# Performance work log

Measured on AMD Instinct MI355X. Metric: run time of the kernel, lower is better.

## Reference

```python
import jax, jax.numpy as jnp
import numpy as np

TARGET_DIM, DRUG_DIM, INT_DIM, HID = 1024, 128, 128, 32
LN_EPS = 1e-5  # torch nn.LayerNorm default (module's eps arg is unused for LN)


def _layernorm(x, g, b):
    mu = jnp.mean(x, axis=-1, keepdims=True)
    var = jnp.var(x, axis=-1, keepdims=True)
    return (x - mu) * jax.lax.rsqrt(var + LN_EPS) * g + b


def setup_inputs() -> dict:
    key = jax.random.key(0)
    ks = jax.random.split(key, 10)
    B, NR, NA = 4, 512, 64
    s_t = 1.0 / np.sqrt(TARGET_DIM)
    s_d = 1.0 / np.sqrt(DRUG_DIM)
    s_o = 1.0 / np.sqrt(HID * HID)
    return {
        "target_embedding": jax.random.normal(ks[0], (B, NR, TARGET_DIM), jnp.float32),
        "drug_embedding": jax.random.normal(ks[1], (B, NA, DRUG_DIM), jnp.float32),
        "target_mask": jnp.ones((B, NR), jnp.float32),
        "drug_mask": jnp.ones((B, NA), jnp.float32),
        "ln_t_g": jnp.ones((TARGET_DIM,), jnp.float32),
        "ln_t_b": jnp.zeros((TARGET_DIM,), jnp.float32),
        "ln_d_g": jnp.ones((DRUG_DIM,), jnp.float32),
        "ln_d_b": jnp.zeros((DRUG_DIM,), jnp.float32),
        "W_t": jax.random.uniform(ks[2], (HID, TARGET_DIM), jnp.float32, -s_t, s_t),
        "b_t": jax.random.uniform(ks[3], (HID,), jnp.float32, -s_t, s_t),
        "W_d": jax.random.uniform(ks[4], (HID, DRUG_DIM), jnp.float32, -s_d, s_d),
        "b_d": jax.random.uniform(ks[5], (HID,), jnp.float32, -s_d, s_d),
        "W_out": jax.random.uniform(ks[6], (INT_DIM, HID * HID), jnp.float32, -s_o, s_o),
        "b_out": jax.random.uniform(ks[7], (INT_DIM,), jnp.float32, -s_o, s_o),
    }


def reference(target_embedding, drug_embedding, target_mask, drug_mask,
              ln_t_g, ln_t_b, ln_d_g, ln_d_b, W_t, b_t, W_d, b_d, W_out, b_out):
    t = _layernorm(target_embedding, ln_t_g, ln_t_b)
    d = _layernorm(drug_embedding, ln_d_g, ln_d_b)
    # projections + mask: [B,NR,H], [B,NA,H]
    tf = (t @ W_t.T + b_t) * target_mask[..., None]
    df = (d @ W_d.T + b_d) * drug_mask[..., None]
    # fused outer-product + linear_out: W_out row index i over flat (c*H+e)
    W3 = W_out.reshape(INT_DIM, HID, HID)  # [i, c, e]
    outer = jnp.einsum('bnc,bme,ice->bnmi', tf, df, W3) + b_out
    mask = target_mask[:, :, None] * drug_mask[:, None, :]  # [B,NR,NA]
    outer = outer * mask[..., None]
    return outer, mask
```

## Files before the change

kernel.cpp:

```cpp
#include <hip/hip_runtime.h>

typedef __attribute__((ext_vector_type(8))) short short8;
typedef __attribute__((ext_vector_type(4))) float f32x4;

#define LNP_YSTRIDE 1032
#define GSTR 1048

__device__ __forceinline__ unsigned short f2bf(float f) {
  union { float f; unsigned u; } v; v.f = f;
  unsigned r = v.u + 0x7FFFu + ((v.u >> 16) & 1u);
  return (unsigned short)(r >> 16);
}
__device__ __forceinline__ unsigned pack2(float a, float b) {
  return (unsigned)f2bf(a) | ((unsigned)f2bf(b) << 16);
}
__device__ __forceinline__ short8 packW(float4 a, float4 b) {
  union { short8 s; unsigned u[4]; } r;
  r.u[0] = pack2(a.x, a.y); r.u[1] = pack2(a.z, a.w);
  r.u[2] = pack2(b.x, b.y); r.u[3] = pack2(b.z, b.w);
  return r.s;
}

template<int ROWLEN>
__device__ __forceinline__ void lnproj(
    const float* __restrict__ X, const float* __restrict__ g, const float* __restrict__ bia,
    const float* __restrict__ W, const float* __restrict__ pb, const float* __restrict__ msk,
    unsigned short* __restrict__ outb, int row0, unsigned short* Yl, float* pd, int tid)
{
  const int w = tid >> 6, lid = tid & 63, l = tid & 15, q = (tid >> 4) & 3;

  #pragma unroll
  for (int rr = 0; rr < 4; ++rr) {
    const int row = w * 4 + rr;
    const float* xr = X + (size_t)(row0 + row) * ROWLEN;
    if (ROWLEN == 1024) {
      float4 v[4];
      float s = 0.f, s2 = 0.f;
      #pragma unroll
      for (int k = 0; k < 4; ++k) {
        v[k] = *(const float4*)(xr + 4 * lid + 256 * k);
        s  += (v[k].x + v[k].y) + (v[k].z + v[k].w);
        s2 += (v[k].x * v[k].x + v[k].y * v[k].y) + (v[k].z * v[k].z + v[k].w * v[k].w);
      }
      #pragma unroll
      for (int off = 32; off >= 1; off >>= 1) { s += __shfl_xor(s, off, 64); s2 += __shfl_xor(s2, off, 64); }
      const float mu = s * (1.f / 1024.f);
      const float rs = rsqrtf(s2 * (1.f / 1024.f) - mu * mu + 1e-5f);
      #pragma unroll
      for (int k = 0; k < 4; ++k) {
        float4 gg = *(const float4*)(g + 4 * lid + 256 * k);
        float4 bb = *(const float4*)(bia + 4 * lid + 256 * k);
        float y0 = (v[k].x - mu) * rs * gg.x + bb.x;
        float y1 = (v[k].y - mu) * rs * gg.y + bb.y;
        float y2 = (v[k].z - mu) * rs * gg.z + bb.z;
        float y3 = (v[k].w - mu) * rs * gg.w + bb.w;
        unsigned* yd = (unsigned*)(Yl + row * LNP_YSTRIDE + 4 * lid + 256 * k);
        yd[0] = pack2(y0, y1); yd[1] = pack2(y2, y3);
      }
    } else {
      float2 v = *(const float2*)(xr + 2 * lid);
      float s = v.x + v.y, s2 = v.x * v.x + v.y * v.y;
      #pragma unroll
      for (int off = 32; off >= 1; off >>= 1) { s += __shfl_xor(s, off, 64); s2 += __shfl_xor(s2, off, 64); }
      const float mu = s * (1.f / 128.f);
      const float rs = rsqrtf(s2 * (1.f / 128.f) - mu * mu + 1e-5f);
      float2 gg = *(const float2*)(g + 2 * lid);
      float2 bb = *(const float2*)(bia + 2 * lid);
      *(unsigned*)(Yl + row * LNP_YSTRIDE + 2 * lid) =
          pack2((v.x - mu) * rs * gg.x + bb.x, (v.y - mu) * rs * gg.y + bb.y);
    }
  }
  __syncthreads();

  const int KST = ROWLEN / 32;
  const int ht = w & 1, kh = w >> 1;
  const int h = ht * 16 + l;
  f32x4 acc = {0.f, 0.f, 0.f, 0.f};
  #pragma unroll
  for (int s = kh * (KST / 2); s < kh * (KST / 2) + KST / 2; ++s) {
    short8 af = *(const short8*)(Yl + l * LNP_YSTRIDE + s * 32 + q * 8);
    const float* wp = W + (size_t)h * ROWLEN + s * 32 + q * 8;
    short8 bf = packW(*(const float4*)wp, *(const float4*)(wp + 4));
    acc = __builtin_amdgcn_mfma_f32_16x16x32_bf16(af, bf, acc, 0, 0, 0);
  }
  if (w >= 2) {
    #pragma unroll
    for (int r = 0; r < 4; ++r) pd[ht * 256 + (q * 4 + r) * 16 + l] = acc[r];
  }
  __syncthreads();
  if (w < 2) {
    const float pbv = pb[h];
    #pragma unroll
    for (int r = 0; r < 4; ++r) {
      const int rg = row0 + q * 4 + r;
      float val = acc[r] + pd[ht * 256 + (q * 4 + r) * 16 + l] + pbv;
      val *= msk[rg];
      outb[(size_t)rg * 32 + h] = f2bf(val);
    }
  }
}

__global__ __launch_bounds__(256) void k_pre(
    const float* __restrict__ tgt, const float* __restrict__ drg,
    const float* __restrict__ tmask, const float* __restrict__ dmask,
    const float* __restrict__ ln_t_g, const float* __restrict__ ln_t_b,
    const float* __restrict__ ln_d_g, const float* __restrict__ ln_d_b,
    const float* __restrict__ W_t, const float* __restrict__ b_t,
    const float* __restrict__ W_d, const float* __restrict__ b_d,
    const float* __restrict__ W_out,
    unsigned short* __restrict__ w3pp, unsigned short* __restrict__ tfb,
    unsigned short* __restrict__ dfb, float* __restrict__ mask_out)
{
  __shared__ unsigned short Yl[16 * LNP_YSTRIDE];
  __shared__ float pd[2 * 16 * 16];
  const int blk = blockIdx.x, tid = threadIdx.x;
  if (blk < 128) {
    lnproj<1024>(tgt, ln_t_g, ln_t_b, W_t, b_t, tmask, tfb, blk * 16, Yl, pd, tid);
  } else if (blk < 144) {
    lnproj<128>(drg, ln_d_g, ln_d_b, W_d, b_d, dmask, dfb, (blk - 128) * 16, Yl, pd, tid);
  } else if (blk < 152) {
    const int tg = (blk - 144) * 256 + tid;
    #pragma unroll
    for (int rep = 0; rep < 2; ++rep) {
      const int f = tg + rep * 2048;
      const int i = f >> 5, e = f & 31;
      unsigned short us[32];
      #pragma unroll
      for (int c = 0; c < 32; ++c) us[c] = f2bf(W_out[i * 1024 + c * 32 + e]);
      unsigned* dst = (unsigned*)(w3pp + (size_t)f * 32);
      #pragma unroll
      for (int j = 0; j < 16; ++j) dst[j] = (unsigned)us[2 * j] | ((unsigned)us[2 * j + 1] << 16);
    }
  } else {
    const int base = ((blk - 152) * 256 + tid) * 4;
    const int b = base >> 15;
    const float tm = tmask[base >> 6];
    float4 d = *(const float4*)(dmask + b * 64 + (base & 63));
    float4 o; o.x = tm * d.x; o.y = tm * d.y; o.z = tm * d.z; o.w = tm * d.w;
    *(float4*)(mask_out + base) = o;
  }
}

__global__ __launch_bounds__(256) void k_main(
    const unsigned short* __restrict__ w3pp, const unsigned short* __restrict__ tfb,
    const unsigned short* __restrict__ dfb, const float* __restrict__ b_out,
    const float* __restrict__ tmask, const float* __restrict__ dmask,
    float* __restrict__ out)
{
  __shared__ unsigned short Gl[16 * GSTR];
  const int id = blockIdx.x;
  const int b = id >> 7, n16 = (id >> 2) & 31, iq = id & 3;
  const int n0 = n16 * 16, i0 = iq * 32;
  const int tid = threadIdx.x, w = tid >> 6, l = tid & 15, q = (tid >> 4) & 3;

  short8 atf = *(const short8*)(tfb + (size_t)(b * 512 + n0 + l) * 32 + q * 8);
  short8 adf[4];
  #pragma unroll
  for (int mt = 0; mt < 4; ++mt)
    adf[mt] = *(const short8*)(dfb + (size_t)(b * 64 + mt * 16 + l) * 32 + q * 8);

  const f32x4 zero = {0.f, 0.f, 0.f, 0.f};

  for (int t = w * 16; t < w * 16 + 16; ++t) {
    const int f = i0 * 32 + t * 16 + l;
    short8 bw = *(const short8*)(w3pp + (size_t)f * 32 + q * 8);
    f32x4 d = __builtin_amdgcn_mfma_f32_16x16x32_bf16(atf, bw, zero, 0, 0, 0);
    const int floc = t * 16 + l, ip = floc >> 5, e = floc & 31;
    #pragma unroll
    for (int r = 0; r < 4; ++r)
      Gl[(q * 4 + r) * GSTR + ip * 32 + e] = f2bf(d[r]);
  }
  __syncthreads();

  const float bo0 = b_out[i0 + l], bo1 = b_out[i0 + 16 + l];

  for (int j = 0; j < 8; ++j) {
    const int p = w * 8 + j, n = p >> 1, it = p & 1;
    short8 bg = *(const short8*)(Gl + n * GSTR + (it * 16 + l) * 32 + q * 8);
    const float tmv = tmask[b * 512 + n0 + n];
    const float bo = it ? bo1 : bo0;
    const size_t obase = ((size_t)(b * 512 + n0 + n) * 64) * 128 + (size_t)(i0 + it * 16 + l);
    #pragma unroll
    for (int mt = 0; mt < 4; ++mt) {
      f32x4 d = __builtin_amdgcn_mfma_f32_16x16x32_bf16(adf[mt], bg, zero, 0, 0, 0);
      #pragma unroll
      for (int r = 0; r < 4; ++r) {
        const int m = mt * 16 + q * 4 + r;
        out[obase + (size_t)m * 128] = (d[r] + bo) * (tmv * dmask[b * 64 + m]);
      }
    }
  }
}

extern "C" void kernel_launch(void* const* d_in, const int* in_sizes, int n_in,
                              void* d_out, int out_size, void* d_ws, size_t ws_size,
                              hipStream_t stream)
{
  const float* tgt    = (const float*)d_in[0];
  const float* drg    = (const float*)d_in[1];
  const float* tmask  = (const float*)d_in[2];
  const float* dmask  = (const float*)d_in[3];
  const float* ln_t_g = (const float*)d_in[4];
  const float* ln_t_b = (const float*)d_in[5];
  const float* ln_d_g = (const float*)d_in[6];
  const float* ln_d_b = (const float*)d_in[7];
  const float* W_t    = (const float*)d_in[8];
  const float* b_t    = (const float*)d_in[9];
  const float* W_d    = (const float*)d_in[10];
  const float* b_d    = (const float*)d_in[11];
  const float* W_out  = (const float*)d_in[12];
  const float* b_out  = (const float*)d_in[13];

  float* out = (float*)d_out;
  float* mask_out = out + (size_t)4 * 512 * 64 * 128;

  char* ws = (char*)d_ws;
  unsigned short* w3pp = (unsigned short*)(ws);
  unsigned short* tfb  = (unsigned short*)(ws + 262144);
  unsigned short* dfb  = (unsigned short*)(ws + 262144 + 131072);

  k_pre<<<dim3(280), dim3(256), 0, stream>>>(
      tgt, drg, tmask, dmask, ln_t_g, ln_t_b, ln_d_g, ln_d_b,
      W_t, b_t, W_d, b_d, W_out, w3pp, tfb, dfb, mask_out);
  k_main<<<dim3(512), dim3(256), 0, stream>>>(
      w3pp, tfb, dfb, b_out, tmask, dmask, out);
}
```

Baseline: 116.5 us.

## Vectorize output stores via swapped MFMA operands and rebalance preprocessing blocks

The second-stage MFMA now takes the G tile as the A operand and the drug features as B. Each lane therefore holds four consecutive interaction outputs and writes them with one float4 store instead of four scalar strided stores, and b_out and dmask are loaded up front. The pre-kernel's LayerNorm+projection now handles 8 rows per block instead of 16, doubling the block count. The W_out repack is spread over 16 blocks, and the combined mask output moves into the main kernel. The aim is fewer store instructions on the dominant output write and better occupancy in the pre-kernel, at the cost of the MFMA computing 8 unused garbage rows per projection block.

Result: slower. 119.6 us (+2.6%).

```diff
diff --git a/kernel.cpp b/kernel.cpp
--- a/kernel.cpp
+++ b/kernel.cpp
@@ -3,7 +3,7 @@
 typedef __attribute__((ext_vector_type(8))) short short8;
 typedef __attribute__((ext_vector_type(4))) float f32x4;
 
-#define LNP_YSTRIDE 1032
+#define YSTR 1032
 #define GSTR 1048
 
 __device__ __forceinline__ unsigned short f2bf(float f) {
@@ -22,7 +22,7 @@
 }
 
 template<int ROWLEN>
-__device__ __forceinline__ void lnproj(
+__device__ __forceinline__ void lnproj8(
     const float* __restrict__ X, const float* __restrict__ g, const float* __restrict__ bia,
     const float* __restrict__ W, const float* __restrict__ pb, const float* __restrict__ msk,
     unsigned short* __restrict__ outb, int row0, unsigned short* Yl, float* pd, int tid)
@@ -30,8 +30,8 @@
   const int w = tid >> 6, lid = tid & 63, l = tid & 15, q = (tid >> 4) & 3;
 
   #pragma unroll
-  for (int rr = 0; rr < 4; ++rr) {
-    const int row = w * 4 + rr;
+  for (int rr = 0; rr < 2; ++rr) {
+    const int row = w * 2 + rr;
     const float* xr = X + (size_t)(row0 + row) * ROWLEN;
     if (ROWLEN == 1024) {
       float4 v[4];
@@ -50,12 +50,9 @@
       for (int k = 0; k < 4; ++k) {
         float4 gg = *(const float4*)(g + 4 * lid + 256 * k);
         float4 bb = *(const float4*)(bia + 4 * lid + 256 * k);
-        float y0 = (v[k].x - mu) * rs * gg.x + bb.x;
-        float y1 = (v[k].y - mu) * rs * gg.y + bb.y;
-        float y2 = (v[k].z - mu) * rs * gg.z + bb.z;
-        float y3 = (v[k].w - mu) * rs * gg.w + bb.w;
-        unsigned* yd = (unsigned*)(Yl + row * LNP_YSTRIDE + 4 * lid + 256 * k);
-        yd[0] = pack2(y0, y1); yd[1] = pack2(y2, y3);
+        unsigned* yd = (unsigned*)(Yl + row * YSTR + 4 * lid + 256 * k);
+        yd[0] = pack2((v[k].x - mu) * rs * gg.x + bb.x, (v[k].y - mu) * rs * gg.y + bb.y);
+        yd[1] = pack2((v[k].z - mu) * rs * gg.z + bb.z, (v[k].w - mu) * rs * gg.w + bb.w);
       }
     } else {
       float2 v = *(const float2*)(xr + 2 * lid);
@@ -66,7 +63,7 @@
       const float rs = rsqrtf(s2 * (1.f / 128.f) - mu * mu + 1e-5f);
       float2 gg = *(const float2*)(g + 2 * lid);
       float2 bb = *(const float2*)(bia + 2 * lid);
-      *(unsigned*)(Yl + row * LNP_YSTRIDE + 2 * lid) =
+      *(unsigned*)(Yl + row * YSTR + 2 * lid) =
           pack2((v.x - mu) * rs * gg.x + bb.x, (v.y - mu) * rs * gg.y + bb.y);
     }
   }
@@ -78,24 +75,23 @@
   f32x4 acc = {0.f, 0.f, 0.f, 0.f};
   #pragma unroll
   for (int s = kh * (KST / 2); s < kh * (KST / 2) + KST / 2; ++s) {
-    short8 af = *(const short8*)(Yl + l * LNP_YSTRIDE + s * 32 + q * 8);
+    short8 af = *(const short8*)(Yl + l * YSTR + s * 32 + q * 8);
     const float* wp = W + (size_t)h * ROWLEN + s * 32 + q * 8;
     short8 bf = packW(*(const float4*)wp, *(const float4*)(wp + 4));
     acc = __builtin_amdgcn_mfma_f32_16x16x32_bf16(af, bf, acc, 0, 0, 0);
   }
-  if (w >= 2) {
-    #pragma unroll
-    for (int r = 0; r < 4; ++r) pd[ht * 256 + (q * 4 + r) * 16 + l] = acc[r];
+  if (kh == 1 && q < 2) {
+    #pragma unroll
+    for (int r = 0; r < 4; ++r) pd[ht * 128 + (q * 4 + r) * 16 + l] = acc[r];
   }
   __syncthreads();
-  if (w < 2) {
+  if (kh == 0 && q < 2) {
     const float pbv = pb[h];
     #pragma unroll
     for (int r = 0; r < 4; ++r) {
-      const int rg = row0 + q * 4 + r;
-      float val = acc[r] + pd[ht * 256 + (q * 4 + r) * 16 + l] + pbv;
-      val *= msk[rg];
-      outb[(size_t)rg * 32 + h] = f2bf(val);
+      const int rl = q * 4 + r, rg = row0 + rl;
+      float val = acc[r] + pd[ht * 128 + rl * 16 + l] + pbv;
+      outb[(size_t)rg * 32 + h] = f2bf(val * msk[rg]);
     }
   }
 }
@@ -109,35 +105,24 @@
     const float* __restrict__ W_d, const float* __restrict__ b_d,
     const float* __restrict__ W_out,
     unsigned short* __restrict__ w3pp, unsigned short* __restrict__ tfb,
-    unsigned short* __restrict__ dfb, float* __restrict__ mask_out)
-{
-  __shared__ unsigned short Yl[16 * LNP_YSTRIDE];
-  __shared__ float pd[2 * 16 * 16];
+    unsigned short* __restrict__ dfb)
+{
+  __shared__ unsigned short Yl[16 * YSTR];
+  __shared__ float pd[2 * 8 * 16];
   const int blk = blockIdx.x, tid = threadIdx.x;
-  if (blk < 128) {
-    lnproj<1024>(tgt, ln_t_g, ln_t_b, W_t, b_t, tmask, tfb, blk * 16, Yl, pd, tid);
-  } else if (blk < 144) {
-    lnproj<128>(drg, ln_d_g, ln_d_b, W_d, b_d, dmask, dfb, (blk - 128) * 16, Yl, pd, tid);
-  } else if (blk < 152) {
-    const int tg = (blk - 144) * 256 + tid;
-    #pragma unroll
-    for (int rep = 0; rep < 2; ++rep) {
-      const int f = tg + rep * 2048;
-      const int i = f >> 5, e = f & 31;
-      unsigned short us[32];
-      #pragma unroll
-      for (int c = 0; c < 32; ++c) us[c] = f2bf(W_out[i * 1024 + c * 32 + e]);
-      unsigned* dst = (unsigned*)(w3pp + (size_t)f * 32);
-      #pragma unroll
-      for (int j = 0; j < 16; ++j) dst[j] = (unsigned)us[2 * j] | ((unsigned)us[2 * j + 1] << 16);
-    }
+  if (blk < 256) {
+    lnproj8<1024>(tgt, ln_t_g, ln_t_b, W_t, b_t, tmask, tfb, blk * 8, Yl, pd, tid);
+  } else if (blk < 288) {
+    lnproj8<128>(drg, ln_d_g, ln_d_b, W_d, b_d, dmask, dfb, (blk - 256) * 8, Yl, pd, tid);
   } else {
-    const int base = ((blk - 152) * 256 + tid) * 4;
-    const int b = base >> 15;
-    const float tm = tmask[base >> 6];
-    float4 d = *(const float4*)(dmask + b * 64 + (base & 63));
-    float4 o; o.x = tm * d.x; o.y = tm * d.y; o.z = tm * d.z; o.w = tm * d.w;
-    *(float4*)(mask_out + base) = o;
+    const int f = (blk - 288) * 256 + tid;
+    const int i = f >> 5, e = f & 31;
+    unsigned short us[32];
+    #pragma unroll
+    for (int c = 0; c < 32; ++c) us[c] = f2bf(W_out[i * 1024 + c * 32 + e]);
+    unsigned* dst = (unsigned*)(w3pp + (size_t)f * 32);
+    #pragma unroll
+    for (int j = 0; j < 16; ++j) dst[j] = (unsigned)us[2 * j] | ((unsigned)us[2 * j + 1] << 16);
   }
 }
 
@@ -145,7 +130,7 @@
     const unsigned short* __restrict__ w3pp, const unsigned short* __restrict__ tfb,
     const unsigned short* __restrict__ dfb, const float* __restrict__ b_out,
     const float* __restrict__ tmask, const float* __restrict__ dmask,
-    float* __restrict__ out)
+    float* __restrict__ out, float* __restrict__ mask_out)
 {
   __shared__ unsigned short Gl[16 * GSTR];
   const int id = blockIdx.x;
@@ -154,40 +139,55 @@
   const int tid = threadIdx.x, w = tid >> 6, l = tid & 15, q = (tid >> 4) & 3;
 
   short8 atf = *(const short8*)(tfb + (size_t)(b * 512 + n0 + l) * 32 + q * 8);
-  short8 adf[4];
+  short8 bdf[4];
   #pragma unroll
   for (int mt = 0; mt < 4; ++mt)
-    adf[mt] = *(const short8*)(dfb + (size_t)(b * 64 + mt * 16 + l) * 32 + q * 8);
+    bdf[mt] = *(const short8*)(dfb + (size_t)(b * 64 + mt * 16 + l) * 32 + q * 8);
 
   const f32x4 zero = {0.f, 0.f, 0.f, 0.f};
 
-  for (int t = w * 16; t < w * 16 + 16; ++t) {
-    const int f = i0 * 32 + t * 16 + l;
-    short8 bw = *(const short8*)(w3pp + (size_t)f * 32 + q * 8);
+  #pragma unroll 8
+  for (int t = 0; t < 16; ++t) {
+    const int tt = w * 16 + t;
+    short8 bw = *(const short8*)(w3pp + (size_t)(i0 * 32 + tt * 16 + l) * 32 + q * 8);
     f32x4 d = __builtin_amdgcn_mfma_f32_16x16x32_bf16(atf, bw, zero, 0, 0, 0);
-    const int floc = t * 16 + l, ip = floc >> 5, e = floc & 31;
+    const int floc = tt * 16 + l, ip = floc >> 5, e = floc & 31;
     #pragma unroll
     for (int r = 0; r < 4; ++r)
       Gl[(q * 4 + r) * GSTR + ip * 32 + e] = f2bf(d[r]);
   }
   __syncthreads();
 
-  const float bo0 = b_out[i0 + l], bo1 = b_out[i0 + 16 + l];
+  const float4 bo0 = *(const float4*)(b_out + i0 + q * 4);
+  const float4 bo1 = *(const float4*)(b_out + i0 + 16 + q * 4);
+  float dm[4];
+  #pragma unroll
+  for (int mt = 0; mt < 4; ++mt) dm[mt] = dmask[b * 64 + mt * 16 + l];
 
   for (int j = 0; j < 8; ++j) {
     const int p = w * 8 + j, n = p >> 1, it = p & 1;
-    short8 bg = *(const short8*)(Gl + n * GSTR + (it * 16 + l) * 32 + q * 8);
+    short8 ag = *(const short8*)(Gl + n * GSTR + (it * 16 + l) * 32 + q * 8);
     const float tmv = tmask[b * 512 + n0 + n];
-    const float bo = it ? bo1 : bo0;
-    const size_t obase = ((size_t)(b * 512 + n0 + n) * 64) * 128 + (size_t)(i0 + it * 16 + l);
+    const float4 bo = it ? bo1 : bo0;
+    const size_t obase = ((size_t)(b * 512 + n0 + n) * 64) * 128 + (size_t)(i0 + it * 16 + q * 4);
     #pragma unroll
     for (int mt = 0; mt < 4; ++mt) {
-      f32x4 d = __builtin_amdgcn_mfma_f32_16x16x32_bf16(adf[mt], bg, zero, 0, 0, 0);
-      #pragma unroll
-      for (int r = 0; r < 4; ++r) {
-        const int m = mt * 16 + q * 4 + r;
-        out[obase + (size_t)m * 128] = (d[r] + bo) * (tmv * dmask[b * 64 + m]);
-      }
+      f32x4 d = __builtin_amdgcn_mfma_f32_16x16x32_bf16(ag, bdf[mt], zero, 0, 0, 0);
+      const float s = tmv * dm[mt];
+      float4 o;
+      o.x = (d[0] + bo.x) * s; o.y = (d[1] + bo.y) * s;
+      o.z = (d[2] + bo.z) * s; o.w = (d[3] + bo.w) * s;
+      *(float4*)(out + obase + (size_t)(mt * 16 + l) * 128) = o;
+    }
+  }
+
+  if (iq == 0) {
+    #pragma unroll
+    for (int k = 0; k < 4; ++k) {
+      const int t = tid + k * 256;
+      const int n = t >> 6, m = t & 63;
+      mask_out[(size_t)(b * 512 + n0 + n) * 64 + m] =
+          tmask[b * 512 + n0 + n] * dmask[b * 64 + m];
     }
   }
 }
@@ -219,9 +219,9 @@
   unsigned short* tfb  = (unsigned short*)(ws + 262144);
   unsigned short* dfb  = (unsigned short*)(ws + 262144 + 131072);
 
-  k_pre<<<dim3(280), dim3(256), 0, stream>>>(
+  k_pre<<<dim3(304), dim3(256), 0, stream>>>(
       tgt, drg, tmask, dmask, ln_t_g, ln_t_b, ln_d_g, ln_d_b,
-      W_t, b_t, W_d, b_d, W_out, w3pp, tfb, dfb, mask_out);
+      W_t, b_t, W_d, b_d, W_out, w3pp, tfb, dfb);
   k_main<<<dim3(512), dim3(256), 0, stream>>>(
-      w3pp, tfb, dfb, b_out, tmask, dmask, out);
-}
+      w3pp, tfb, dfb, b_out, tmask, dmask, out, mask_out);
+}
```
